# Kernel optimization log

Hardware: AMD Instinct MI355X
Metric: run time of the kernel (lower is better)

The kernel has to match this reference:

```python
import jax, jax.numpy as jnp
import numpy as np

H = 128          # input hidden dim
HID = 128        # expert hidden width
OUT = 128        # out_channels
NR = 8           # n_routed
NS = 2           # n_shared
RDIM = 16        # router feature dim


def setup_inputs() -> dict:
    key = jax.random.key(0)
    ks = jax.random.split(key, 11)
    s = 0.05
    x = jax.random.normal(ks[0], (2, 32, 32, 32, H), dtype=jnp.float32)
    # router params
    Wr1 = jax.random.normal(ks[1], (H, RDIM), dtype=jnp.float32) * s
    br1 = jnp.zeros((RDIM,), dtype=jnp.float32)
    Wr2 = jax.random.normal(ks[2], (RDIM, NR), dtype=jnp.float32) * s
    br2 = jnp.zeros((NR,), dtype=jnp.float32)
    # routed expert params, stacked on leading expert axis
    We1 = jax.random.normal(ks[3], (NR, H, HID), dtype=jnp.float32) * s
    be1 = jnp.zeros((NR, HID), dtype=jnp.float32)
    We2 = jax.random.normal(ks[4], (NR, HID, OUT), dtype=jnp.float32) * s
    be2 = jnp.zeros((NR, OUT), dtype=jnp.float32)
    # shared expert params
    Ws1 = jax.random.normal(ks[5], (NS, H, HID), dtype=jnp.float32) * s
    bs1 = jnp.zeros((NS, HID), dtype=jnp.float32)
    Ws2 = jax.random.normal(ks[6], (NS, HID, OUT), dtype=jnp.float32) * s
    bs2 = jnp.zeros((NS, OUT), dtype=jnp.float32)
    return dict(x=x, Wr1=Wr1, br1=br1, Wr2=Wr2, br2=br2,
                We1=We1, be1=be1, We2=We2, be2=be2,
                Ws1=Ws1, bs1=bs1, Ws2=Ws2, bs2=bs2)


def reference(x, Wr1, br1, Wr2, br2, We1, be1, We2, be2, Ws1, bs1, Ws2, bs2):
    # router: Dense(16) -> relu -> Dense(n_routed) -> softmax
    rf = jax.nn.relu(jnp.einsum('...h,hr->...r', x, Wr1) + br1)
    logits = jnp.einsum('...r,re->...e', rf, Wr2) + br2
    gate = jax.nn.softmax(logits, axis=-1)                      # [..., NR]
    threshold = 1.0 / NR
    mask = (gate > threshold).astype(gate.dtype)
    mg = gate * mask
    mg = mg / (jnp.sum(mg, axis=-1, keepdims=True) + 1e-8)
    # routed experts (batched over expert axis e): Dense -> gelu(tanh) -> Dense
    hr = jax.nn.gelu(jnp.einsum('...h,ehd->...ed', x, We1) + be1)   # [..., NR, HID]
    ro = jnp.einsum('...ed,edo->...eo', hr, We2) + be2              # [..., NR, OUT]
    routed_agg = jnp.einsum('...eo,...e->...o', ro, mg)
    # shared experts summed
    hs = jax.nn.gelu(jnp.einsum('...h,ehd->...ed', x, Ws1) + bs1)   # [..., NS, HID]
    so = jnp.einsum('...ed,edo->...eo', hs, Ws2) + bs2              # [..., NS, OUT]
    shared_agg = jnp.sum(so, axis=-2)
    return routed_agg + shared_agg
```

## Files before the change

### kernel.cpp

```cpp
#include <hip/hip_runtime.h>
#include <hip/hip_bf16.h>

typedef __bf16 bf16x8 __attribute__((ext_vector_type(8)));
typedef float  f32x16 __attribute__((ext_vector_type(16)));
typedef float  f32x4  __attribute__((ext_vector_type(4)));
typedef float  f32x2  __attribute__((ext_vector_type(2)));

static __device__ __forceinline__ f32x16 mfma32(bf16x8 a, bf16x8 b, f32x16 c) {
    return __builtin_amdgcn_mfma_f32_32x32x16_bf16(a, b, c, 0, 0, 0);
}

static __device__ __forceinline__ void gl_lds16(const void* g, void* l) {
    __builtin_amdgcn_global_load_lds(
        (const __attribute__((address_space(1))) unsigned int*)g,
        (__attribute__((address_space(3))) unsigned int*)l,
        16, 0, 0);
}

#define GELU_C1 2.30220820f
#define GELU_C2 0.10294324f

static __device__ __forceinline__ bf16x8 gelu8(f32x16 a, int base, float gv) {
    bf16x8 r;
    #pragma unroll
    for (int p = 0; p < 4; ++p) {
        f32x2 hh; hh[0] = a[base + 2 * p]; hh[1] = a[base + 2 * p + 1];
        f32x2 tt = hh * hh;
        f32x2 pp;
        pp[0] = fmaf(tt[0], -GELU_C2, -GELU_C1);
        pp[1] = fmaf(tt[1], -GELU_C2, -GELU_C1);
        f32x2 mm = hh * pp;
        float e0 = __builtin_amdgcn_exp2f(mm[0]);
        float e1 = __builtin_amdgcn_exp2f(mm[1]);
        float q0 = __builtin_amdgcn_rcpf(1.f + e0);
        float q1 = __builtin_amdgcn_rcpf(1.f + e1);
        r[2 * p]     = (__bf16)(hh[0] * q0 * gv);
        r[2 * p + 1] = (__bf16)(hh[1] * q1 * gv);
    }
    return r;
}

__global__ __launch_bounds__(256) void pack_kernel(
    const float* __restrict__ We1, const float* __restrict__ be1,
    const float* __restrict__ Ws1, const float* __restrict__ bs1,
    const float* __restrict__ We2, const float* __restrict__ Ws2,
    const float* __restrict__ Wr1, const float* __restrict__ br1,
    const float* __restrict__ Wr2, const float* __restrict__ br2,
    __bf16* __restrict__ w1p, __bf16* __restrict__ w2p,
    float* __restrict__ be1p,
    double* __restrict__ wr1d, double* __restrict__ br1d,
    double* __restrict__ wr2d, double* __restrict__ br2d)
{
    int tid = blockIdx.x * 256 + threadIdx.x;
    if (tid < 20480) {
        int l  = tid & 63;
        int ks = (tid >> 6) & 7;
        int nt = (tid >> 9) & 3;
        int e  = tid >> 11;
        const float* src = (e < 8) ? (We1 + e * 16384) : (Ws1 + (e - 8) * 16384);
        int n  = nt * 32 + (l & 31);
        int kb = ks * 16 + (l >> 5) * 8;
        bf16x8 v;
        #pragma unroll
        for (int j = 0; j < 8; ++j) v[j] = (__bf16)src[(kb + j) * 128 + n];
        *(bf16x8*)(w1p + (size_t)tid * 8) = v;
    } else if (tid < 40960) {
        int t2 = tid - 20480;
        int l  = t2 & 63;
        int ot = (t2 >> 6) & 3;
        int kq = (t2 >> 8) & 7;
        int e  = t2 >> 11;
        const float* src = (e < 8) ? (We2 + e * 16384) : (Ws2 + (e - 8) * 16384);
        int o  = 32 * ot + (l & 31);
        int lh = l >> 5;
        bf16x8 v;
        #pragma unroll
        for (int j = 0; j < 8; ++j) {
            int hid = 16 * kq + 8 * (j >> 2) + 4 * lh + (j & 3);
            v[j] = (__bf16)src[hid * 128 + o];
        }
        *(bf16x8*)(w2p + (size_t)t2 * 8) = v;
    } else if (tid < 42240) {
        int i  = tid - 40960;
        int r  = i & 15;
        int h2 = (i >> 4) & 1;
        int nt = (i >> 5) & 3;
        int e  = i >> 7;
        int n  = 32 * nt + (r & 3) + 8 * (r >> 2) + 4 * h2;
        be1p[i] = (e < 8) ? be1[e * 128 + n] : bs1[(e - 8) * 128 + n];
    } else if (tid < 44288) {
        int i = tid - 42240;
        wr1d[i] = (double)Wr1[i];
    } else if (tid < 44416) {
        int i = tid - 44288;
        wr2d[i] = (double)Wr2[i];
    } else if (tid < 44432) {
        int i = tid - 44416;
        br1d[i] = (double)br1[i];
    } else if (tid < 44440) {
        int i = tid - 44432;
        br2d[i] = (double)br2[i];
    }
}

__global__ __launch_bounds__(256) void router_kernel(
    const float* __restrict__ x,
    const double* __restrict__ wr1d, const double* __restrict__ br1d,
    const double* __restrict__ wr2d, const double* __restrict__ br2d,
    float* __restrict__ gates)
{
    __shared__ __align__(16) char lds[41472];
    float*  xs  = (float*)lds;
    double* rfs = (double*)(lds + 33280);

    const int t    = threadIdx.x;
    const int tok0 = blockIdx.x * 64;

    #pragma unroll
    for (int i = 0; i < 8; ++i) {
        int cid = i * 256 + t;
        int m = cid >> 5;
        int c = cid & 31;
        f32x4 v = *(const f32x4*)(x + (size_t)(tok0 + m) * 128 + c * 4);
        f32x2 s0, s1;
        s0[0] = v[0]; s0[1] = v[1]; s1[0] = v[2]; s1[1] = v[3];
        *(f32x2*)(xs + m * 130 + c * 4)     = s0;
        *(f32x2*)(xs + m * 130 + c * 4 + 2) = s1;
    }
    __syncthreads();

    {
        const int tok = t & 63;
        const int rq  = (t >> 6) * 4;
        const int rqs = __builtin_amdgcn_readfirstlane(rq);
        double rf4[4];
        #pragma unroll
        for (int j = 0; j < 4; ++j) rf4[j] = br1d[rqs + j];
        const float* xr = xs + tok * 130;
        #pragma unroll 4
        for (int c = 0; c < 64; ++c) {
            f32x2 xv2 = *(const f32x2*)(xr + c * 2);
            #pragma unroll
            for (int q = 0; q < 2; ++q) {
                double xv = (double)xv2[q];
                int k = c * 2 + q;
                #pragma unroll
                for (int j = 0; j < 4; ++j)
                    rf4[j] = fma(xv, wr1d[k * 16 + rqs + j], rf4[j]);
            }
        }
        #pragma unroll
        for (int j = 0; j < 4; ++j)
            rfs[tok * 16 + rq + j] = rf4[j] > 0.0 ? rf4[j] : 0.0;
    }
    __syncthreads();

    if (t < 64) {
        double lg[8];
        #pragma unroll
        for (int j = 0; j < 8; ++j) lg[j] = br2d[j];
        #pragma unroll
        for (int r = 0; r < 16; ++r) {
            double rv = rfs[t * 16 + r];
            #pragma unroll
            for (int j = 0; j < 8; ++j)
                lg[j] = fma(rv, wr2d[r * 8 + j], lg[j]);
        }
        double mx = lg[0];
        #pragma unroll
        for (int j = 1; j < 8; ++j) mx = lg[j] > mx ? lg[j] : mx;
        double ex[8]; double s = 0.0;
        #pragma unroll
        for (int j = 0; j < 8; ++j) { ex[j] = exp(lg[j] - mx); s += ex[j]; }
        double ms = 0.0;
        bool mk[8];
        #pragma unroll
        for (int j = 0; j < 8; ++j) {
            mk[j] = (8.0 * ex[j] > s);
            ms += mk[j] ? ex[j] : 0.0;
        }
        double inv = 1.0 / (ms + s * 1e-8);
        f32x4 o0, o1;
        #pragma unroll
        for (int j = 0; j < 4; ++j) {
            o0[j] = mk[j]     ? (float)(ex[j] * inv)     : 0.f;
            o1[j] = mk[4 + j] ? (float)(ex[4 + j] * inv) : 0.f;
        }
        *(f32x4*)(gates + (size_t)(tok0 + t) * 8)     = o0;
        *(f32x4*)(gates + (size_t)(tok0 + t) * 8 + 4) = o1;
    }
}

#define GEMM2_STEP(W)                                   \
    acc0 = mfma32(h0, W[0], acc0);                      \
    acc1 = mfma32(h0, W[1], acc1);                      \
    acc2 = mfma32(h0, W[2], acc2);                      \
    acc3 = mfma32(h0, W[3], acc3);                      \
    acc0 = mfma32(h1, W[4], acc0);                      \
    acc1 = mfma32(h1, W[5], acc1);                      \
    acc2 = mfma32(h1, W[6], acc2);                      \
    acc3 = mfma32(h1, W[7], acc3);

__global__ __launch_bounds__(512, 2) void moe_main_kernel(
    const float* __restrict__ x, const float* __restrict__ gates,
    const __bf16* __restrict__ w1p, const __bf16* __restrict__ w2p,
    const float* __restrict__ be1p,
    const float* __restrict__ be2, const float* __restrict__ bs2,
    float* __restrict__ out)
{
    __shared__ __align__(16) char lds[131072];

    const int t    = threadIdx.x;
    const int lane = t & 63;
    const int wv   = t >> 6;
    const int l31  = lane & 31;
    const int hi   = lane >> 5;
    const int tok0 = blockIdx.x * 256;
    const size_t row = (size_t)(tok0 + 32 * wv + l31);

    #define FILL_EXPERT(buf, e)                                                 \
    {                                                                           \
        const char* g1 = (const char*)(w1p + (size_t)(e) * 16384)               \
                         + wv * 4096 + lane * 16;                               \
        const char* g2 = (const char*)(w2p + (size_t)(e) * 16384)               \
                         + wv * 4096 + lane * 16;                               \
        char* l1 = lds + (buf) * 65536 + wv * 4096;                             \
        char* l2 = lds + (buf) * 65536 + 32768 + wv * 4096;                     \
        _Pragma("unroll")                                                       \
        for (int i = 0; i < 4; ++i) {                                           \
            gl_lds16(g1 + i * 1024, l1 + i * 1024);                             \
            gl_lds16(g2 + i * 1024, l2 + i * 1024);                             \
        }                                                                       \
    }

    FILL_EXPERT(0, 0)

    bf16x8 xf[8];
    {
        const float* xr = x + row * 128 + 8 * hi;
        #pragma unroll
        for (int ks = 0; ks < 8; ++ks) {
            f32x4 va = *(const f32x4*)(xr + 16 * ks);
            f32x4 vb = *(const f32x4*)(xr + 16 * ks + 4);
            bf16x8 v;
            v[0]=(__bf16)va[0]; v[1]=(__bf16)va[1]; v[2]=(__bf16)va[2]; v[3]=(__bf16)va[3];
            v[4]=(__bf16)vb[0]; v[5]=(__bf16)vb[1]; v[6]=(__bf16)vb[2]; v[7]=(__bf16)vb[3];
            xf[ks] = v;
        }
    }

    f32x16 acc0, acc1, acc2, acc3;
    #pragma unroll
    for (int i = 0; i < 16; ++i) { acc0[i]=0.f; acc1[i]=0.f; acc2[i]=0.f; acc3[i]=0.f; }

    asm volatile("s_waitcnt vmcnt(0)" ::: "memory");
    __builtin_amdgcn_s_barrier();
    __builtin_amdgcn_sched_barrier(0);

    int cur = 0;
    #pragma unroll 1
    for (int e = 0; e < 10; ++e) {
        if (e < 9) FILL_EXPERT(cur ^ 1, e + 1)

        const bf16x8* W1L = (const bf16x8*)(lds + cur * 65536);
        const bf16x8* W2L = (const bf16x8*)(lds + cur * 65536 + 32768);

        float gv = 1.0f;
        if (e < 8) gv = gates[row * 8 + e];

        #pragma unroll
        for (int nt = 0; nt < 4; ++nt) {
            bf16x8 wb[8];
            #pragma unroll
            for (int ks = 0; ks < 8; ++ks) wb[ks] = W1L[(nt * 8 + ks) * 64 + lane];

            const f32x16 bfr = *(const f32x16*)(be1p + ((e * 4 + nt) * 2 + hi) * 16);

            __builtin_amdgcn_s_setprio(1);
            f32x16 a;
            #pragma unroll
            for (int i = 0; i < 16; ++i) a[i] = 0.f;
            #pragma unroll
            for (int ks = 0; ks < 8; ++ks) a = mfma32(wb[ks], xf[ks], a);
            __builtin_amdgcn_s_setprio(0);

            a += bfr;
            bf16x8 h0 = gelu8(a, 0, gv);
            bf16x8 h1 = gelu8(a, 8, gv);

            bf16x8 wB[8];
            #pragma unroll
            for (int f = 0; f < 8; ++f) wB[f] = W2L[(2 * nt * 4 + f) * 64 + lane];

            __builtin_amdgcn_s_setprio(1);
            GEMM2_STEP(wB)
            __builtin_amdgcn_s_setprio(0);
        }

        asm volatile("s_waitcnt vmcnt(0)" ::: "memory");
        __builtin_amdgcn_s_barrier();
        __builtin_amdgcn_sched_barrier(0);
        cur ^= 1;
    }

    {
        float be2c[4][8], bsc[4];
        #pragma unroll
        for (int ot = 0; ot < 4; ++ot) {
            int o = 32 * ot + l31;
            bsc[ot] = bs2[o] + bs2[128 + o];
            #pragma unroll
            for (int ee = 0; ee < 8; ++ee) be2c[ot][ee] = be2[ee * 128 + o];
        }
        #pragma unroll
        for (int r = 0; r < 16; ++r) {
            int mrow = (r & 3) + 8 * (r >> 2) + 4 * hi;
            size_t trow = (size_t)(tok0 + 32 * wv + mrow);
            f32x4 g0 = *(const f32x4*)(gates + trow * 8);
            f32x4 g1 = *(const f32x4*)(gates + trow * 8 + 4);
            size_t obase = trow * 128 + l31;
            #pragma unroll
            for (int ot = 0; ot < 4; ++ot) {
                float b = bsc[ot];
                #pragma unroll
                for (int ee = 0; ee < 4; ++ee) b = fmaf(g0[ee], be2c[ot][ee], b);
                #pragma unroll
                for (int ee = 0; ee < 4; ++ee) b = fmaf(g1[ee], be2c[ot][4 + ee], b);
                float av = (ot == 0) ? acc0[r] : (ot == 1) ? acc1[r]
                         : (ot == 2) ? acc2[r] : acc3[r];
                out[obase + 32 * ot] = av + b;
            }
        }
    }
    #undef FILL_EXPERT
}

extern "C" void kernel_launch(void* const* d_in, const int* in_sizes, int n_in,
                              void* d_out, int out_size, void* d_ws, size_t ws_size,
                              hipStream_t stream)
{
    const float* x   = (const float*)d_in[0];
    const float* Wr1 = (const float*)d_in[1];
    const float* br1 = (const float*)d_in[2];
    const float* Wr2 = (const float*)d_in[3];
    const float* br2 = (const float*)d_in[4];
    const float* We1 = (const float*)d_in[5];
    const float* be1 = (const float*)d_in[6];
    const float* We2 = (const float*)d_in[7];
    const float* be2 = (const float*)d_in[8];
    const float* Ws1 = (const float*)d_in[9];
    const float* bs1 = (const float*)d_in[10];
    const float* Ws2 = (const float*)d_in[11];
    const float* bs2 = (const float*)d_in[12];

    __bf16* w1p  = (__bf16*)d_ws;
    __bf16* w2p  = (__bf16*)((char*)d_ws + 327680);
    float*  be1p = (float*)((char*)d_ws + 655360);
    double* wr1d = (double*)((char*)d_ws + 660480);
    double* wr2d = (double*)((char*)d_ws + 676864);
    double* br1d = (double*)((char*)d_ws + 677888);
    double* br2d = (double*)((char*)d_ws + 678016);
    float*  gts  = (float*)((char*)d_ws + 720896);

    pack_kernel<<<174, 256, 0, stream>>>(We1, be1, Ws1, bs1, We2, Ws2,
                                         Wr1, br1, Wr2, br2,
                                         w1p, w2p, be1p, wr1d, br1d, wr2d, br2d);
    router_kernel<<<1024, 256, 0, stream>>>(x, wr1d, br1d, wr2d, br2d, gts);
    moe_main_kernel<<<256, 512, 0, stream>>>(x, gts, w1p, w2p, be1p, be2, bs2,
                                             (float*)d_out);
}
```

Measured before the change: 179.9 us.

## Shrink MoE blocks to 256 threads with single-buffered LDS and prefetched weights

The main kernel now runs 512 blocks of 256 threads, each covering 128 tokens. LDS drops to one 64KB buffer per expert instead of a 128KB double buffer, so more blocks can be resident per CU. The expert fill is no longer overlapped with compute: each expert's weights load after a barrier and are waited on. Inside the loop, W1 fragments for the next tile are prefetched before the GELU, W2 fragments load before GEMM1, and GEMM1 is split into two accumulator chains with the bias folded into the initial value. The risk is exposed load latency per expert in exchange for higher occupancy and more latency hiding across blocks.

```diff
diff --git a/kernel.cpp b/kernel.cpp
--- a/kernel.cpp
+++ b/kernel.cpp
@@ -201,39 +201,39 @@
     acc2 = mfma32(h1, W[6], acc2);                      \
     acc3 = mfma32(h1, W[7], acc3);
 
-__global__ __launch_bounds__(512, 2) void moe_main_kernel(
+__global__ __launch_bounds__(256, 2) void moe_main_kernel(
     const float* __restrict__ x, const float* __restrict__ gates,
     const __bf16* __restrict__ w1p, const __bf16* __restrict__ w2p,
     const float* __restrict__ be1p,
     const float* __restrict__ be2, const float* __restrict__ bs2,
     float* __restrict__ out)
 {
-    __shared__ __align__(16) char lds[131072];
+    __shared__ __align__(16) char lds[65536];
 
     const int t    = threadIdx.x;
     const int lane = t & 63;
     const int wv   = t >> 6;
     const int l31  = lane & 31;
     const int hi   = lane >> 5;
-    const int tok0 = blockIdx.x * 256;
+    const int tok0 = blockIdx.x * 128;
     const size_t row = (size_t)(tok0 + 32 * wv + l31);
 
-    #define FILL_EXPERT(buf, e)                                                 \
+    #define FILL_EXPERT(e)                                                      \
     {                                                                           \
         const char* g1 = (const char*)(w1p + (size_t)(e) * 16384)               \
-                         + wv * 4096 + lane * 16;                               \
+                         + wv * 8192 + lane * 16;                               \
         const char* g2 = (const char*)(w2p + (size_t)(e) * 16384)               \
-                         + wv * 4096 + lane * 16;                               \
-        char* l1 = lds + (buf) * 65536 + wv * 4096;                             \
-        char* l2 = lds + (buf) * 65536 + 32768 + wv * 4096;                     \
+                         + wv * 8192 + lane * 16;                               \
+        char* l1 = lds + wv * 8192;                                             \
+        char* l2 = lds + 32768 + wv * 8192;                                     \
         _Pragma("unroll")                                                       \
-        for (int i = 0; i < 4; ++i) {                                           \
+        for (int i = 0; i < 8; ++i) {                                           \
             gl_lds16(g1 + i * 1024, l1 + i * 1024);                             \
             gl_lds16(g2 + i * 1024, l2 + i * 1024);                             \
         }                                                                       \
     }
 
-    FILL_EXPERT(0, 0)
+    FILL_EXPERT(0)
 
     bf16x8 xf[8];
     {
@@ -253,54 +253,65 @@
     #pragma unroll
     for (int i = 0; i < 16; ++i) { acc0[i]=0.f; acc1[i]=0.f; acc2[i]=0.f; acc3[i]=0.f; }
 
+    const bf16x8* W1L = (const bf16x8*)(lds);
+    const bf16x8* W2L = (const bf16x8*)(lds + 32768);
+
     asm volatile("s_waitcnt vmcnt(0)" ::: "memory");
     __builtin_amdgcn_s_barrier();
     __builtin_amdgcn_sched_barrier(0);
 
-    int cur = 0;
     #pragma unroll 1
     for (int e = 0; e < 10; ++e) {
-        if (e < 9) FILL_EXPERT(cur ^ 1, e + 1)
-
-        const bf16x8* W1L = (const bf16x8*)(lds + cur * 65536);
-        const bf16x8* W2L = (const bf16x8*)(lds + cur * 65536 + 32768);
-
         float gv = 1.0f;
         if (e < 8) gv = gates[row * 8 + e];
 
+        bf16x8 wb[8];
+        #pragma unroll
+        for (int ks = 0; ks < 8; ++ks) wb[ks] = W1L[ks * 64 + lane];
+
         #pragma unroll
         for (int nt = 0; nt < 4; ++nt) {
-            bf16x8 wb[8];
-            #pragma unroll
-            for (int ks = 0; ks < 8; ++ks) wb[ks] = W1L[(nt * 8 + ks) * 64 + lane];
+            bf16x8 wB[8];
+            #pragma unroll
+            for (int f = 0; f < 8; ++f) wB[f] = W2L[(8 * nt + f) * 64 + lane];
 
             const f32x16 bfr = *(const f32x16*)(be1p + ((e * 4 + nt) * 2 + hi) * 16);
 
             __builtin_amdgcn_s_setprio(1);
-            f32x16 a;
-            #pragma unroll
-            for (int i = 0; i < 16; ++i) a[i] = 0.f;
-            #pragma unroll
-            for (int ks = 0; ks < 8; ++ks) a = mfma32(wb[ks], xf[ks], a);
+            f32x16 alo = bfr;
+            f32x16 ahi;
+            #pragma unroll
+            for (int i = 0; i < 16; ++i) ahi[i] = 0.f;
+            #pragma unroll
+            for (int ks = 0; ks < 4; ++ks) {
+                alo = mfma32(wb[ks],     xf[ks],     alo);
+                ahi = mfma32(wb[ks + 4], xf[ks + 4], ahi);
+            }
             __builtin_amdgcn_s_setprio(0);
 
-            a += bfr;
+            if (nt < 3) {
+                #pragma unroll
+                for (int ks = 0; ks < 8; ++ks)
+                    wb[ks] = W1L[((nt + 1) * 8 + ks) * 64 + lane];
+            }
+
+            f32x16 a = alo + ahi;
             bf16x8 h0 = gelu8(a, 0, gv);
             bf16x8 h1 = gelu8(a, 8, gv);
-
-            bf16x8 wB[8];
-            #pragma unroll
-            for (int f = 0; f < 8; ++f) wB[f] = W2L[(2 * nt * 4 + f) * 64 + lane];
 
             __builtin_amdgcn_s_setprio(1);
             GEMM2_STEP(wB)
             __builtin_amdgcn_s_setprio(0);
         }
 
-        asm volatile("s_waitcnt vmcnt(0)" ::: "memory");
         __builtin_amdgcn_s_barrier();
         __builtin_amdgcn_sched_barrier(0);
-        cur ^= 1;
+        if (e < 9) {
+            FILL_EXPERT(e + 1)
+            asm volatile("s_waitcnt vmcnt(0)" ::: "memory");
+            __builtin_amdgcn_s_barrier();
+            __builtin_amdgcn_sched_barrier(0);
+        }
     }
 
     {
@@ -366,6 +377,6 @@
                                          Wr1, br1, Wr2, br2,
                                          w1p, w2p, be1p, wr1d, br1d, wr2d, br2d);
     router_kernel<<<1024, 256, 0, stream>>>(x, wr1d, br1d, wr2d, br2d, gts);
-    moe_main_kernel<<<256, 512, 0, stream>>>(x, gts, w1p, w2p, be1p, be2, bs2,
+    moe_main_kernel<<<512, 256, 0, stream>>>(x, gts, w1p, w2p, be1p, be2, bs2,
                                              (float*)d_out);
 }
```

After: 185.4 us. 3.0% more time.
